# Performance work log

Hardware: AMD Instinct MI355X
Metric: run time of the kernel (lower is better)

Reference implementation:

```python
import jax, jax.numpy as jnp
import numpy as np
from jax import lax

SIGMA = 1.0
ALPHA = 1.0
BETA = 1.0
TRUNCATE = 4.0  # scipy.ndimage default


def _gauss_kernel(sigma):
    radius = int(TRUNCATE * sigma + 0.5)  # scipy radius rule -> 4 for sigma=1
    x = np.arange(-radius, radius + 1, dtype=np.float64)
    k = np.exp(-0.5 * (x / sigma) ** 2)
    k = (k / k.sum()).astype(np.float32)
    return k

_KERNEL = _gauss_kernel(SIGMA)


def _blur_axis(img, k, axis):
    # scipy mode='reflect' == jnp.pad mode='symmetric' (edge repeated)
    r = len(k) // 2
    pad = [(0, 0)] * img.ndim
    pad[axis] = (r, r)
    xp = jnp.pad(img, pad, mode='symmetric')
    n = img.shape[axis]
    out = k[0] * lax.slice_in_dim(xp, 0, n, axis=axis)
    for i in range(1, len(k)):
        out = out + k[i] * lax.slice_in_dim(xp, i, i + n, axis=axis)
    return out


def gaussian_blur(img):
    # scalar sigma in scipy blurs along EVERY axis, including batch & channel
    k = jnp.asarray(_KERNEL, dtype=img.dtype)
    for ax in range(img.ndim):
        img = _blur_axis(img, k, ax)
    return img


def decompose(I):
    I_log = jnp.log(I + 1e-6)
    I_smooth = gaussian_blur(I_log)
    R = I_log - I_smooth
    L = I_log - R  # == I_smooth
    return jnp.exp(L), jnp.exp(R)


def setup_inputs() -> dict:
    key = jax.random.key(0)
    k1, k2 = jax.random.split(key)
    shape = (16, 3, 512, 512)
    I_enhanced = jax.random.uniform(k1, shape, dtype=jnp.float32)
    I_gt = jax.random.uniform(k2, shape, dtype=jnp.float32)
    return {"I_enhanced": I_enhanced, "I_gt": I_gt}


def reference(I_enhanced, I_gt):
    L_enh, R_enh = decompose(I_enhanced)
    L_gt, R_gt = decompose(I_gt)
    L_reflectance = jnp.mean((R_enh - R_gt) ** 2)
    L_illumination = jnp.mean((L_enh - L_gt) ** 2)
    return ALPHA * L_reflectance + BETA * L_illumination
```

## Files before the change

### kernel.cpp

```cpp
#include <hip/hip_runtime.h>
#include <hip/hip_fp16.h>
#include <cmath>

#define PLANE (512*512)
#define NPLANES 48
#define NEL (48*PLANE)

struct Taps { float k[9]; };
struct CMat { float w[3][3]; };


__global__ __launch_bounds__(64)
void k_blur_hw(const float* __restrict__ inE, const float* __restrict__ inG,
               ushort* __restrict__ wsS, ushort* __restrict__ wsI, Taps tp)
{
    const int l    = threadIdx.x;
    const int w0   = (blockIdx.x & 1) * 256;
    const int r0   = (blockIdx.x >> 1) * 32;
    const int z    = blockIdx.y;

    const float* src = (z < NPLANES) ? (inE + z * PLANE)
                                     : (inG + (z - NPLANES) * PLANE);

    const int  col   = w0 + 4 * l;
    const bool is0   = (l == 0);
    const bool is63  = (l == 63);
    const bool ledge = (w0 == 0);
    const bool redge = (w0 + 256 == 512);
    const bool do_halo = (is0 && !ledge) || (is63 && !redge);
    const int  hoff  = is0 ? (w0 - 4) : (w0 + 256);
    const int  tile  = col >> 6;
    const int  inner = col & 63;

    __half2 kh[9];
#pragma unroll
    for (int t = 0; t < 9; ++t) kh[t] = __float2half2_rn(tp.k[t]);

    __half2 ring[10][2];

#define FOLD(r) ((r) < 0 ? (-1 - (r)) : ((r) > 511 ? (1023 - (r)) : (r)))

    float4 pown[3], phal[3];
    phal[0] = phal[1] = phal[2] = make_float4(1.f, 1.f, 1.f, 1.f);
#pragma unroll
    for (int s = 0; s < 3; ++s) {
        const float* rp = src + FOLD(r0 - 4 + s) * 512;
        pown[s] = *(const float4*)(rp + col);
        if (do_halo) phal[s] = *(const float4*)(rp + hoff);
    }

    for (int jb = 0; jb < 40; jb += 10) {
#pragma unroll
        for (int u = 0; u < 10; ++u) {
            const int j = jb + u;

            float4 own = pown[0], hal = phal[0];
            pown[0] = pown[1]; pown[1] = pown[2];
            phal[0] = phal[1]; phal[1] = phal[2];
            if (j + 3 < 40) {
                const float* rp = src + FOLD(r0 - 1 + j) * 512;
                pown[2] = *(const float4*)(rp + col);
                if (do_halo) phal[2] = *(const float4*)(rp + hoff);
            }

            if (j >= 4 && j < 36) {
                const int ri = r0 + j - 4;
                __half2 i0 = __floats2half2_rn(own.x + 1e-6f, own.y + 1e-6f);
                __half2 i1 = __floats2half2_rn(own.z + 1e-6f, own.w + 1e-6f);
                ushort* dpI = wsI + (((ri * 8 + tile) * 96) + z) * 64 + inner;
                *(uint2*)dpI = make_uint2(*(uint*)&i0, *(uint*)&i1);
            }

            const float w4 = __logf(own.x + 1e-6f);
            const float w5 = __logf(own.y + 1e-6f);
            const float w6 = __logf(own.z + 1e-6f);
            const float w7 = __logf(own.w + 1e-6f);
            const float h0 = __logf(hal.x + 1e-6f);
            const float h1 = __logf(hal.y + 1e-6f);
            const float h2 = __logf(hal.z + 1e-6f);
            const float h3 = __logf(hal.w + 1e-6f);

            float win[12];
            win[4] = w4; win[5] = w5; win[6] = w6; win[7] = w7;
            win[0] = __shfl_up(w4, 1);
            win[1] = __shfl_up(w5, 1);
            win[2] = __shfl_up(w6, 1);
            win[3] = __shfl_up(w7, 1);
            win[8]  = __shfl_down(w4, 1);
            win[9]  = __shfl_down(w5, 1);
            win[10] = __shfl_down(w6, 1);
            win[11] = __shfl_down(w7, 1);
            if (is0) {
                if (ledge) { win[0] = w7; win[1] = w6; win[2] = w5; win[3] = w4; }
                else       { win[0] = h0; win[1] = h1; win[2] = h2; win[3] = h3; }
            }
            if (is63) {
                if (redge) { win[8] = w7; win[9] = w6; win[10] = w5; win[11] = w4; }
                else       { win[8] = h0; win[9] = h1; win[10] = h2; win[11] = h3; }
            }

            {
                float o0 = 0.f, o1 = 0.f, o2 = 0.f, o3 = 0.f;
#pragma unroll
                for (int t = 0; t < 9; ++t) {
                    const float kt = tp.k[t];
                    o0 += kt * win[t];
                    o1 += kt * win[t + 1];
                    o2 += kt * win[t + 2];
                    o3 += kt * win[t + 3];
                }
                ring[u][0] = __floats2half2_rn(o0, o1);
                ring[u][1] = __floats2half2_rn(o2, o3);
            }

            if (j >= 8) {
                __half2 a0 = __float2half2_rn(0.f), a1 = a0;
#pragma unroll
                for (int t = 0; t < 9; ++t) {
                    const int sl = (u + 2 + t) % 10;
                    a0 = __hfma2(kh[t], ring[sl][0], a0);
                    a1 = __hfma2(kh[t], ring[sl][1], a1);
                }
                const int ro = r0 + j - 8;
                ushort* dpS = wsS + (((ro * 8 + tile) * 96) + z) * 64 + inner;
                *(uint2*)dpS = make_uint2(*(uint*)&a0, *(uint*)&a1);
            }
        }
    }
#undef FOLD
}

__global__ __launch_bounds__(256)
void k_cn_loss(const ushort* __restrict__ wsS, const ushort* __restrict__ wsI,
               float* __restrict__ out, Taps tp, CMat cm)
{
    const int tid = threadIdx.x;
    const int P   = blockIdx.x * 256 + tid;
    const int hw0 = P * 2;
    const int off = (hw0 >> 6) * (96 * 64) + (hw0 & 63);
    const ushort* sbase = wsS + off;
    const ushort* ibase = wsI + off;

    __half2 k2[9], cw[3][3];
#pragma unroll
    for (int t = 0; t < 9; ++t) k2[t] = __float2half2_rn(tp.k[t]);
#pragma unroll
    for (int i = 0; i < 3; ++i)
#pragma unroll
        for (int j = 0; j < 3; ++j) cw[i][j] = __float2half2_rn(cm.w[i][j]);

    __half2 re[9][3];
    __half2 rg[9][3];

#define LOADRAW(m, uE, uG)                                                     \
    uE[0] = *(const uint*)(sbase + ((m) * 3 + 0) * 64);                        \
    uE[1] = *(const uint*)(sbase + ((m) * 3 + 1) * 64);                        \
    uE[2] = *(const uint*)(sbase + ((m) * 3 + 2) * 64);                        \
    uG[0] = *(const uint*)(sbase + (48 + (m) * 3 + 0) * 64);                   \
    uG[1] = *(const uint*)(sbase + (48 + (m) * 3 + 1) * 64);                   \
    uG[2] = *(const uint*)(sbase + (48 + (m) * 3 + 2) * 64);

#define CBLUR(u, dst)                                                          \
    {                                                                          \
        __half2 v0 = *(__half2*)&u[0];                                         \
        __half2 v1 = *(__half2*)&u[1];                                         \
        __half2 v2 = *(__half2*)&u[2];                                         \
        dst[0] = __hfma2(cw[0][0], v0, __hfma2(cw[0][1], v1, __hmul2(cw[0][2], v2))); \
        dst[1] = __hfma2(cw[1][0], v0, __hfma2(cw[1][1], v1, __hmul2(cw[1][2], v2))); \
        dst[2] = __hfma2(cw[2][0], v0, __hfma2(cw[2][1], v1, __hmul2(cw[2][2], v2))); \
    }

#pragma unroll
    for (int m = 0; m < 4; ++m) {
        uint uE[3], uG[3];
        LOADRAW(m, uE, uG);
        CBLUR(uE, re[m]); CBLUR(uG, rg[m]);
    }
    uint nuE[3], nuG[3];
    LOADRAW(4, nuE, nuG);
    uint ieq[3], igq[3];
#pragma unroll
    for (int c = 0; c < 3; ++c) {
        ieq[c] = *(const uint*)(ibase + c * 64);
        igq[c] = *(const uint*)(ibase + (48 + c) * 64);
    }

    float acc = 0.f;
#pragma unroll
    for (int n = 0; n < 16; ++n) {
        uint nie[3], nig[3];
        if (n + 1 < 16) {
#pragma unroll
            for (int c = 0; c < 3; ++c) {
                nie[c] = *(const uint*)(ibase + (((n + 1) * 3 + c)) * 64);
                nig[c] = *(const uint*)(ibase + ((48 + (n + 1) * 3 + c)) * 64);
            }
        }
        const int mnew = n + 4;
        if (mnew < 16) {
            CBLUR(nuE, re[mnew % 9]); CBLUR(nuG, rg[mnew % 9]);
            if (mnew + 1 < 16) { LOADRAW(mnew + 1, nuE, nuG); }
        }
#pragma unroll
        for (int c = 0; c < 3; ++c) {
            __half2 se2 = __float2half2_rn(0.f), sg2 = se2;
#pragma unroll
            for (int t = 0; t < 9; ++t) {
                int m = n - 4 + t;
                m = (m < 0) ? (-1 - m) : ((m > 15) ? (31 - m) : m);
                se2 = __hfma2(k2[t], re[m % 9][c], se2);
                sg2 = __hfma2(k2[t], rg[m % 9][c], sg2);
            }
            const float2 sef = __half22float2(se2);
            const float2 sgf = __half22float2(sg2);
            const float2 ief = __half22float2(*(__half2*)&ieq[c]);
            const float2 igf = __half22float2(*(__half2*)&igq[c]);

            {
                float ee = __expf(-sef.x), eg = __expf(-sgf.x);
                float Re = ief.x * ee;
                float Rg = igf.x * eg;
                float Le = __builtin_amdgcn_rcpf(ee);
                float Lg = __builtin_amdgcn_rcpf(eg);
                float dr = Re - Rg, dl = Le - Lg;
                acc += dr * dr + dl * dl;
            }
            {
                float ee = __expf(-sef.y), eg = __expf(-sgf.y);
                float Re = ief.y * ee;
                float Rg = igf.y * eg;
                float Le = __builtin_amdgcn_rcpf(ee);
                float Lg = __builtin_amdgcn_rcpf(eg);
                float dr = Re - Rg, dl = Le - Lg;
                acc += dr * dr + dl * dl;
            }
        }
        if (n + 1 < 16) {
#pragma unroll
            for (int c = 0; c < 3; ++c) { ieq[c] = nie[c]; igq[c] = nig[c]; }
        }
    }
#undef LOADRAW
#undef CBLUR

    __shared__ float red[256];
    red[tid] = acc;
    __syncthreads();
#pragma unroll
    for (int s = 128; s > 0; s >>= 1) {
        if (tid < s) red[tid] += red[tid + s];
        __syncthreads();
    }
    if (tid == 0) atomicAdd(out, red[0] * (1.0f / (float)NEL));
}

extern "C" void kernel_launch(void* const* d_in, const int* in_sizes, int n_in,
                              void* d_out, int out_size, void* d_ws, size_t ws_size,
                              hipStream_t stream) {
    const float* Ie = (const float*)d_in[0];
    const float* Ig = (const float*)d_in[1];

    Taps tp;
    {
        double kk[9], s = 0.0;
        for (int i = 0; i < 9; ++i) { double x = (double)(i - 4); kk[i] = exp(-0.5 * x * x); s += kk[i]; }
        for (int i = 0; i < 9; ++i) tp.k[i] = (float)(kk[i] / s);
    }

    CMat cm;
    {
        for (int c = 0; c < 3; ++c) {
            cm.w[c][0] = cm.w[c][1] = cm.w[c][2] = 0.f;
            for (int t = 0; t < 9; ++t) {
                int m = c - 4 + t;
                int mm = ((m % 6) + 6) % 6;
                if (mm > 2) mm = 5 - mm;
                cm.w[c][mm] += tp.k[t];
            }
        }
    }

    ushort* wsS = (ushort*)d_ws;
    ushort* wsI = wsS + 2 * (size_t)NEL;

    hipMemsetAsync(d_out, 0, sizeof(float), stream);
    dim3 g1(32, 96);
    k_blur_hw<<<g1, 64, 0, stream>>>(Ie, Ig, wsS, wsI, tp);
    k_cn_loss<<<512, 256, 0, stream>>>(wsS, wsI, (float*)d_out, tp, cm);
}
```

Before: 166.3 us.

## Pair enhanced/gt values in half2 and share row halos via LDS

The first kernel now processes the enhanced and ground-truth planes together, with 128 threads covering a full 512-wide row and 16 rows per block. Horizontal neighbours are exchanged through double-buffered shared memory instead of shuffles and separately loaded halo columns. Workspace entries pack the E and G values of one pixel into a single half2, so the loss kernel does one load and one blur per pair and maps one thread per pixel over twice as many blocks. This removes the redundant halo loads and the duplicated E/G address streams, at the cost of a __syncthreads per row and shorter row strips, which add more vertical halo rows per block.

```diff
diff --git a/kernel.cpp b/kernel.cpp
--- a/kernel.cpp
+++ b/kernel.cpp
@@ -10,136 +10,152 @@
 struct CMat { float w[3][3]; };
 
 
-__global__ __launch_bounds__(64)
+#define FOLD(r) ((r) < 0 ? (-1 - (r)) : ((r) > 511 ? (1023 - (r)) : (r)))
+
+__global__ __launch_bounds__(128)
 void k_blur_hw(const float* __restrict__ inE, const float* __restrict__ inG,
-               ushort* __restrict__ wsS, ushort* __restrict__ wsI, Taps tp)
+               uint* __restrict__ wsS, uint* __restrict__ wsI, Taps tp)
 {
-    const int l    = threadIdx.x;
-    const int w0   = (blockIdx.x & 1) * 256;
-    const int r0   = (blockIdx.x >> 1) * 32;
-    const int z    = blockIdx.y;
-
-    const float* src = (z < NPLANES) ? (inE + z * PLANE)
-                                     : (inG + (z - NPLANES) * PLANE);
-
-    const int  col   = w0 + 4 * l;
-    const bool is0   = (l == 0);
-    const bool is63  = (l == 63);
-    const bool ledge = (w0 == 0);
-    const bool redge = (w0 + 256 == 512);
-    const bool do_halo = (is0 && !ledge) || (is63 && !redge);
-    const int  hoff  = is0 ? (w0 - 4) : (w0 + 256);
-    const int  tile  = col >> 6;
-    const int  inner = col & 63;
+    const int g  = threadIdx.x;
+    const int r0 = blockIdx.x * 16;
+    const int z  = blockIdx.y;
+    const float* __restrict__ srcE = inE + z * PLANE;
+    const float* __restrict__ srcG = inG + z * PLANE;
+    const int col   = 4 * g;
+    const int tile  = col >> 6;
+    const int inner = col & 63;
+    const bool edge = (g == 0) || (g == 127);
+    const int  eoff = (g == 0) ? 0 : 516;
+
+    __shared__ float buf[2][2][520];
 
     __half2 kh[9];
 #pragma unroll
     for (int t = 0; t < 9; ++t) kh[t] = __float2half2_rn(tp.k[t]);
 
-    __half2 ring[10][2];
-
-#define FOLD(r) ((r) < 0 ? (-1 - (r)) : ((r) > 511 ? (1023 - (r)) : (r)))
-
-    float4 pown[3], phal[3];
-    phal[0] = phal[1] = phal[2] = make_float4(1.f, 1.f, 1.f, 1.f);
+    __half2 ring[12][4];
+
+    float4 pE[3], pG[3];
 #pragma unroll
     for (int s = 0; s < 3; ++s) {
-        const float* rp = src + FOLD(r0 - 4 + s) * 512;
-        pown[s] = *(const float4*)(rp + col);
-        if (do_halo) phal[s] = *(const float4*)(rp + hoff);
-    }
-
-    for (int jb = 0; jb < 40; jb += 10) {
-#pragma unroll
-        for (int u = 0; u < 10; ++u) {
-            const int j = jb + u;
-
-            float4 own = pown[0], hal = phal[0];
-            pown[0] = pown[1]; pown[1] = pown[2];
-            phal[0] = phal[1]; phal[1] = phal[2];
-            if (j + 3 < 40) {
-                const float* rp = src + FOLD(r0 - 1 + j) * 512;
-                pown[2] = *(const float4*)(rp + col);
-                if (do_halo) phal[2] = *(const float4*)(rp + hoff);
-            }
-
-            if (j >= 4 && j < 36) {
+        const int row = FOLD(r0 - 4 + s);
+        pE[s] = *(const float4*)(srcE + row * 512 + col);
+        pG[s] = *(const float4*)(srcG + row * 512 + col);
+    }
+
+#pragma unroll
+    for (int jb = 0; jb < 24; jb += 12) {
+#pragma unroll
+        for (int u = 0; u < 12; ++u) {
+            const int j   = jb + u;
+            const int par = j & 1;
+
+            float4 oe = pE[0], og = pG[0];
+            pE[0] = pE[1]; pE[1] = pE[2];
+            pG[0] = pG[1]; pG[1] = pG[2];
+            if (j + 3 < 24) {
+                const int row = FOLD(r0 - 1 + j);
+                pE[2] = *(const float4*)(srcE + row * 512 + col);
+                pG[2] = *(const float4*)(srcG + row * 512 + col);
+            }
+
+            const float e4 = __logf(oe.x + 1e-6f);
+            const float e5 = __logf(oe.y + 1e-6f);
+            const float e6 = __logf(oe.z + 1e-6f);
+            const float e7 = __logf(oe.w + 1e-6f);
+            const float g4 = __logf(og.x + 1e-6f);
+            const float g5 = __logf(og.y + 1e-6f);
+            const float g6 = __logf(og.z + 1e-6f);
+            const float g7 = __logf(og.w + 1e-6f);
+
+            *(float4*)&buf[par][0][4 + col] = make_float4(e4, e5, e6, e7);
+            *(float4*)&buf[par][1][4 + col] = make_float4(g4, g5, g6, g7);
+            if (edge) {
+                *(float4*)&buf[par][0][eoff] = make_float4(e7, e6, e5, e4);
+                *(float4*)&buf[par][1][eoff] = make_float4(g7, g6, g5, g4);
+            }
+
+            if (j >= 4 && j < 20) {
                 const int ri = r0 + j - 4;
-                __half2 i0 = __floats2half2_rn(own.x + 1e-6f, own.y + 1e-6f);
-                __half2 i1 = __floats2half2_rn(own.z + 1e-6f, own.w + 1e-6f);
-                ushort* dpI = wsI + (((ri * 8 + tile) * 96) + z) * 64 + inner;
-                *(uint2*)dpI = make_uint2(*(uint*)&i0, *(uint*)&i1);
-            }
-
-            const float w4 = __logf(own.x + 1e-6f);
-            const float w5 = __logf(own.y + 1e-6f);
-            const float w6 = __logf(own.z + 1e-6f);
-            const float w7 = __logf(own.w + 1e-6f);
-            const float h0 = __logf(hal.x + 1e-6f);
-            const float h1 = __logf(hal.y + 1e-6f);
-            const float h2 = __logf(hal.z + 1e-6f);
-            const float h3 = __logf(hal.w + 1e-6f);
-
-            float win[12];
-            win[4] = w4; win[5] = w5; win[6] = w6; win[7] = w7;
-            win[0] = __shfl_up(w4, 1);
-            win[1] = __shfl_up(w5, 1);
-            win[2] = __shfl_up(w6, 1);
-            win[3] = __shfl_up(w7, 1);
-            win[8]  = __shfl_down(w4, 1);
-            win[9]  = __shfl_down(w5, 1);
-            win[10] = __shfl_down(w6, 1);
-            win[11] = __shfl_down(w7, 1);
-            if (is0) {
-                if (ledge) { win[0] = w7; win[1] = w6; win[2] = w5; win[3] = w4; }
-                else       { win[0] = h0; win[1] = h1; win[2] = h2; win[3] = h3; }
-            }
-            if (is63) {
-                if (redge) { win[8] = w7; win[9] = w6; win[10] = w5; win[11] = w4; }
-                else       { win[8] = h0; win[9] = h1; win[10] = h2; win[11] = h3; }
-            }
-
+                __half2 i0 = __floats2half2_rn(oe.x + 1e-6f, og.x + 1e-6f);
+                __half2 i1 = __floats2half2_rn(oe.y + 1e-6f, og.y + 1e-6f);
+                __half2 i2 = __floats2half2_rn(oe.z + 1e-6f, og.z + 1e-6f);
+                __half2 i3 = __floats2half2_rn(oe.w + 1e-6f, og.w + 1e-6f);
+                uint* dp = wsI + (((ri * 8 + tile) * 48) + z) * 64 + inner;
+                *(uint4*)dp = make_uint4(*(uint*)&i0, *(uint*)&i1,
+                                         *(uint*)&i2, *(uint*)&i3);
+            }
+
+            __syncthreads();
+
+            float oE0, oE1, oE2, oE3, oG0, oG1, oG2, oG3;
             {
+                float4 lA = *(const float4*)&buf[par][0][col];
+                float4 lB = *(const float4*)&buf[par][0][col + 8];
+                float wv[12] = {lA.x, lA.y, lA.z, lA.w, e4, e5, e6, e7,
+                                lB.x, lB.y, lB.z, lB.w};
                 float o0 = 0.f, o1 = 0.f, o2 = 0.f, o3 = 0.f;
 #pragma unroll
                 for (int t = 0; t < 9; ++t) {
                     const float kt = tp.k[t];
-                    o0 += kt * win[t];
-                    o1 += kt * win[t + 1];
-                    o2 += kt * win[t + 2];
-                    o3 += kt * win[t + 3];
+                    o0 += kt * wv[t];
+                    o1 += kt * wv[t + 1];
+                    o2 += kt * wv[t + 2];
+                    o3 += kt * wv[t + 3];
                 }
-                ring[u][0] = __floats2half2_rn(o0, o1);
-                ring[u][1] = __floats2half2_rn(o2, o3);
-            }
+                oE0 = o0; oE1 = o1; oE2 = o2; oE3 = o3;
+            }
+            {
+                float4 lA = *(const float4*)&buf[par][1][col];
+                float4 lB = *(const float4*)&buf[par][1][col + 8];
+                float wv[12] = {lA.x, lA.y, lA.z, lA.w, g4, g5, g6, g7,
+                                lB.x, lB.y, lB.z, lB.w};
+                float o0 = 0.f, o1 = 0.f, o2 = 0.f, o3 = 0.f;
+#pragma unroll
+                for (int t = 0; t < 9; ++t) {
+                    const float kt = tp.k[t];
+                    o0 += kt * wv[t];
+                    o1 += kt * wv[t + 1];
+                    o2 += kt * wv[t + 2];
+                    o3 += kt * wv[t + 3];
+                }
+                oG0 = o0; oG1 = o1; oG2 = o2; oG3 = o3;
+            }
+            ring[u][0] = __floats2half2_rn(oE0, oG0);
+            ring[u][1] = __floats2half2_rn(oE1, oG1);
+            ring[u][2] = __floats2half2_rn(oE2, oG2);
+            ring[u][3] = __floats2half2_rn(oE3, oG3);
 
             if (j >= 8) {
-                __half2 a0 = __float2half2_rn(0.f), a1 = a0;
+                __half2 a0 = __float2half2_rn(0.f), a1 = a0, a2 = a0, a3 = a0;
 #pragma unroll
                 for (int t = 0; t < 9; ++t) {
-                    const int sl = (u + 2 + t) % 10;
+                    const int sl = (j - 8 + t) % 12;
                     a0 = __hfma2(kh[t], ring[sl][0], a0);
                     a1 = __hfma2(kh[t], ring[sl][1], a1);
+                    a2 = __hfma2(kh[t], ring[sl][2], a2);
+                    a3 = __hfma2(kh[t], ring[sl][3], a3);
                 }
                 const int ro = r0 + j - 8;
-                ushort* dpS = wsS + (((ro * 8 + tile) * 96) + z) * 64 + inner;
-                *(uint2*)dpS = make_uint2(*(uint*)&a0, *(uint*)&a1);
-            }
-        }
-    }
-#undef FOLD
+                uint* dp = wsS + (((ro * 8 + tile) * 48) + z) * 64 + inner;
+                *(uint4*)dp = make_uint4(*(uint*)&a0, *(uint*)&a1,
+                                         *(uint*)&a2, *(uint*)&a3);
+            }
+        }
+    }
 }
 
 __global__ __launch_bounds__(256)
-void k_cn_loss(const ushort* __restrict__ wsS, const ushort* __restrict__ wsI,
+void k_cn_loss(const uint* __restrict__ wsS, const uint* __restrict__ wsI,
                float* __restrict__ out, Taps tp, CMat cm)
 {
     const int tid = threadIdx.x;
-    const int P   = blockIdx.x * 256 + tid;
-    const int hw0 = P * 2;
-    const int off = (hw0 >> 6) * (96 * 64) + (hw0 & 63);
-    const ushort* sbase = wsS + off;
-    const ushort* ibase = wsI + off;
+    const int p   = blockIdx.x * 256 + tid;
+    const int w   = p & 511;
+    const int h   = p >> 9;
+    const int base = ((h * 8 + (w >> 6)) * 48) * 64 + (w & 63);
+    const uint* __restrict__ sb = wsS + base;
+    const uint* __restrict__ ib = wsI + base;
 
     __half2 k2[9], cw[3][3];
 #pragma unroll
@@ -147,100 +163,71 @@
 #pragma unroll
     for (int i = 0; i < 3; ++i)
 #pragma unroll
-        for (int j = 0; j < 3; ++j) cw[i][j] = __float2half2_rn(cm.w[i][j]);
-
-    __half2 re[9][3];
-    __half2 rg[9][3];
-
-#define LOADRAW(m, uE, uG)                                                     \
-    uE[0] = *(const uint*)(sbase + ((m) * 3 + 0) * 64);                        \
-    uE[1] = *(const uint*)(sbase + ((m) * 3 + 1) * 64);                        \
-    uE[2] = *(const uint*)(sbase + ((m) * 3 + 2) * 64);                        \
-    uG[0] = *(const uint*)(sbase + (48 + (m) * 3 + 0) * 64);                   \
-    uG[1] = *(const uint*)(sbase + (48 + (m) * 3 + 1) * 64);                   \
-    uG[2] = *(const uint*)(sbase + (48 + (m) * 3 + 2) * 64);
-
-#define CBLUR(u, dst)                                                          \
+        for (int jj = 0; jj < 3; ++jj) cw[i][jj] = __float2half2_rn(cm.w[i][jj]);
+
+    __half2 r[9][3];
+
+#define LOADS(m, u)                                                            \
+    u[0] = sb[((m) * 3 + 0) * 64];                                             \
+    u[1] = sb[((m) * 3 + 1) * 64];                                             \
+    u[2] = sb[((m) * 3 + 2) * 64];
+
+#define CBLUR(u, d)                                                            \
     {                                                                          \
         __half2 v0 = *(__half2*)&u[0];                                         \
         __half2 v1 = *(__half2*)&u[1];                                         \
         __half2 v2 = *(__half2*)&u[2];                                         \
-        dst[0] = __hfma2(cw[0][0], v0, __hfma2(cw[0][1], v1, __hmul2(cw[0][2], v2))); \
-        dst[1] = __hfma2(cw[1][0], v0, __hfma2(cw[1][1], v1, __hmul2(cw[1][2], v2))); \
-        dst[2] = __hfma2(cw[2][0], v0, __hfma2(cw[2][1], v1, __hmul2(cw[2][2], v2))); \
-    }
-
-#pragma unroll
-    for (int m = 0; m < 4; ++m) {
-        uint uE[3], uG[3];
-        LOADRAW(m, uE, uG);
-        CBLUR(uE, re[m]); CBLUR(uG, rg[m]);
-    }
-    uint nuE[3], nuG[3];
-    LOADRAW(4, nuE, nuG);
-    uint ieq[3], igq[3];
-#pragma unroll
-    for (int c = 0; c < 3; ++c) {
-        ieq[c] = *(const uint*)(ibase + c * 64);
-        igq[c] = *(const uint*)(ibase + (48 + c) * 64);
-    }
+        d[0] = __hfma2(cw[0][0], v0, __hfma2(cw[0][1], v1, __hmul2(cw[0][2], v2))); \
+        d[1] = __hfma2(cw[1][0], v0, __hfma2(cw[1][1], v1, __hmul2(cw[1][2], v2))); \
+        d[2] = __hfma2(cw[2][0], v0, __hfma2(cw[2][1], v1, __hmul2(cw[2][2], v2))); \
+    }
+
+    {
+        uint su[3];
+#pragma unroll
+        for (int m = 0; m < 4; ++m) { LOADS(m, su); CBLUR(su, r[m]); }
+    }
+    uint nu[3];
+    LOADS(4, nu);
+    uint iu[3];
+    iu[0] = ib[0]; iu[1] = ib[64]; iu[2] = ib[128];
 
     float acc = 0.f;
 #pragma unroll
     for (int n = 0; n < 16; ++n) {
-        uint nie[3], nig[3];
+        uint niu[3];
         if (n + 1 < 16) {
 #pragma unroll
-            for (int c = 0; c < 3; ++c) {
-                nie[c] = *(const uint*)(ibase + (((n + 1) * 3 + c)) * 64);
-                nig[c] = *(const uint*)(ibase + ((48 + (n + 1) * 3 + c)) * 64);
-            }
+            for (int c = 0; c < 3; ++c) niu[c] = ib[((n + 1) * 3 + c) * 64];
         }
         const int mnew = n + 4;
         if (mnew < 16) {
-            CBLUR(nuE, re[mnew % 9]); CBLUR(nuG, rg[mnew % 9]);
-            if (mnew + 1 < 16) { LOADRAW(mnew + 1, nuE, nuG); }
+            CBLUR(nu, r[mnew % 9]);
+            if (mnew + 1 < 16) { LOADS(mnew + 1, nu); }
         }
 #pragma unroll
         for (int c = 0; c < 3; ++c) {
-            __half2 se2 = __float2half2_rn(0.f), sg2 = se2;
+            __half2 s2 = __float2half2_rn(0.f);
 #pragma unroll
             for (int t = 0; t < 9; ++t) {
                 int m = n - 4 + t;
                 m = (m < 0) ? (-1 - m) : ((m > 15) ? (31 - m) : m);
-                se2 = __hfma2(k2[t], re[m % 9][c], se2);
-                sg2 = __hfma2(k2[t], rg[m % 9][c], sg2);
-            }
-            const float2 sef = __half22float2(se2);
-            const float2 sgf = __half22float2(sg2);
-            const float2 ief = __half22float2(*(__half2*)&ieq[c]);
-            const float2 igf = __half22float2(*(__half2*)&igq[c]);
-
-            {
-                float ee = __expf(-sef.x), eg = __expf(-sgf.x);
-                float Re = ief.x * ee;
-                float Rg = igf.x * eg;
-                float Le = __builtin_amdgcn_rcpf(ee);
-                float Lg = __builtin_amdgcn_rcpf(eg);
-                float dr = Re - Rg, dl = Le - Lg;
-                acc += dr * dr + dl * dl;
-            }
-            {
-                float ee = __expf(-sef.y), eg = __expf(-sgf.y);
-                float Re = ief.y * ee;
-                float Rg = igf.y * eg;
-                float Le = __builtin_amdgcn_rcpf(ee);
-                float Lg = __builtin_amdgcn_rcpf(eg);
-                float dr = Re - Rg, dl = Le - Lg;
-                acc += dr * dr + dl * dl;
-            }
-        }
-        if (n + 1 < 16) {
-#pragma unroll
-            for (int c = 0; c < 3; ++c) { ieq[c] = nie[c]; igq[c] = nig[c]; }
-        }
-    }
-#undef LOADRAW
+                s2 = __hfma2(k2[t], r[m % 9][c], s2);
+            }
+            const float2 sf  = __half22float2(s2);
+            const float2 if2 = __half22float2(*(__half2*)&iu[c]);
+
+            float eE = __expf(-sf.x), eG = __expf(-sf.y);
+            float Re = if2.x * eE;
+            float Rg = if2.y * eG;
+            float Le = __builtin_amdgcn_rcpf(eE);
+            float Lg = __builtin_amdgcn_rcpf(eG);
+            float dr = Re - Rg, dl = Le - Lg;
+            acc += dr * dr + dl * dl;
+        }
+        if (n + 1 < 16) { iu[0] = niu[0]; iu[1] = niu[1]; iu[2] = niu[2]; }
+    }
+#undef LOADS
 #undef CBLUR
 
     __shared__ float red[256];
@@ -280,11 +267,11 @@
         }
     }
 
-    ushort* wsS = (ushort*)d_ws;
-    ushort* wsI = wsS + 2 * (size_t)NEL;
+    uint* wsS = (uint*)d_ws;
+    uint* wsI = wsS + (size_t)NEL;
 
     hipMemsetAsync(d_out, 0, sizeof(float), stream);
-    dim3 g1(32, 96);
-    k_blur_hw<<<g1, 64, 0, stream>>>(Ie, Ig, wsS, wsI, tp);
-    k_cn_loss<<<512, 256, 0, stream>>>(wsS, wsI, (float*)d_out, tp, cm);
+    dim3 g1(32, 48);
+    k_blur_hw<<<g1, 128, 0, stream>>>(Ie, Ig, wsS, wsI, tp);
+    k_cn_loss<<<1024, 256, 0, stream>>>(wsS, wsI, (float*)d_out, tp, cm);
 }
```

Result: slower. 176.8 us (+6.3%).

## Restructure HW blur: full-row wavefront, 8 columns per lane, packed half2 horizontal pass

Applied to the files above, without the earlier changes.

The horizontal+vertical blur kernel now has one wavefront cover a full 512-wide row, with 8 columns per lane. This removes the halo loads and the two-half-row split, and row strips shrink from 32 to 16 rows. The horizontal 9-tap pass now runs in packed half2 on log values. Neighbour values are assembled by shuffling and bit-repacking half pairs, with lane pairs interleaving columns c and c+4. Stores widen to 16 bytes. In exchange, the vertical halo is re-read more often because strips are shorter, the horizontal pass loses precision in fp16, and edge reflection depends on bit-manipulation packing that has to be correct.

```diff
diff --git a/kernel.cpp b/kernel.cpp
--- a/kernel.cpp
+++ b/kernel.cpp
@@ -9,125 +9,130 @@
 struct Taps { float k[9]; };
 struct CMat { float w[3][3]; };
 
+
+#define FOLD(r) ((r) < 0 ? (-1 - (r)) : ((r) > 511 ? (1023 - (r)) : (r)))
 
 __global__ __launch_bounds__(64)
 void k_blur_hw(const float* __restrict__ inE, const float* __restrict__ inG,
                ushort* __restrict__ wsS, ushort* __restrict__ wsI, Taps tp)
 {
-    const int l    = threadIdx.x;
-    const int w0   = (blockIdx.x & 1) * 256;
-    const int r0   = (blockIdx.x >> 1) * 32;
-    const int z    = blockIdx.y;
-
-    const float* src = (z < NPLANES) ? (inE + z * PLANE)
-                                     : (inG + (z - NPLANES) * PLANE);
-
-    const int  col   = w0 + 4 * l;
-    const bool is0   = (l == 0);
-    const bool is63  = (l == 63);
-    const bool ledge = (w0 == 0);
-    const bool redge = (w0 + 256 == 512);
-    const bool do_halo = (is0 && !ledge) || (is63 && !redge);
-    const int  hoff  = is0 ? (w0 - 4) : (w0 + 256);
-    const int  tile  = col >> 6;
-    const int  inner = col & 63;
+    const int l  = threadIdx.x;
+    const int r0 = blockIdx.x * 16;
+    const int z  = blockIdx.y;
+    const float* __restrict__ src = (z < NPLANES) ? (inE + z * PLANE)
+                                                  : (inG + (z - NPLANES) * PLANE);
+    const int col  = 8 * l;
+    const int tile = l >> 3;
+    const int sh   = (l & 7) * 8;
 
     __half2 kh[9];
 #pragma unroll
     for (int t = 0; t < 9; ++t) kh[t] = __float2half2_rn(tp.k[t]);
 
-    __half2 ring[10][2];
-
-#define FOLD(r) ((r) < 0 ? (-1 - (r)) : ((r) > 511 ? (1023 - (r)) : (r)))
-
-    float4 pown[3], phal[3];
-    phal[0] = phal[1] = phal[2] = make_float4(1.f, 1.f, 1.f, 1.f);
+    uint ring[12][4];
+
+    float4 pA[3], pB[3];
 #pragma unroll
     for (int s = 0; s < 3; ++s) {
-        const float* rp = src + FOLD(r0 - 4 + s) * 512;
-        pown[s] = *(const float4*)(rp + col);
-        if (do_halo) phal[s] = *(const float4*)(rp + hoff);
-    }
-
-    for (int jb = 0; jb < 40; jb += 10) {
-#pragma unroll
-        for (int u = 0; u < 10; ++u) {
+        const int row = FOLD(r0 - 4 + s);
+        pA[s] = *(const float4*)(src + row * 512 + col);
+        pB[s] = *(const float4*)(src + row * 512 + col + 4);
+    }
+
+    for (int jb = 0; jb < 24; jb += 12) {
+#pragma unroll
+        for (int u = 0; u < 12; ++u) {
             const int j = jb + u;
 
-            float4 own = pown[0], hal = phal[0];
-            pown[0] = pown[1]; pown[1] = pown[2];
-            phal[0] = phal[1]; phal[1] = phal[2];
-            if (j + 3 < 40) {
-                const float* rp = src + FOLD(r0 - 1 + j) * 512;
-                pown[2] = *(const float4*)(rp + col);
-                if (do_halo) phal[2] = *(const float4*)(rp + hoff);
-            }
-
-            if (j >= 4 && j < 36) {
+            const float4 a = pA[0], b = pB[0];
+            pA[0] = pA[1]; pA[1] = pA[2];
+            pB[0] = pB[1]; pB[1] = pB[2];
+            if (j + 3 < 24) {
+                const int row = FOLD(r0 - 1 + j);
+                pA[2] = *(const float4*)(src + row * 512 + col);
+                pB[2] = *(const float4*)(src + row * 512 + col + 4);
+            }
+
+            const float a0 = a.x + 1e-6f, a1 = a.y + 1e-6f;
+            const float a2 = a.z + 1e-6f, a3 = a.w + 1e-6f;
+            const float b0 = b.x + 1e-6f, b1 = b.y + 1e-6f;
+            const float b2 = b.z + 1e-6f, b3 = b.w + 1e-6f;
+
+            if (j >= 4 && j < 20) {
                 const int ri = r0 + j - 4;
-                __half2 i0 = __floats2half2_rn(own.x + 1e-6f, own.y + 1e-6f);
-                __half2 i1 = __floats2half2_rn(own.z + 1e-6f, own.w + 1e-6f);
-                ushort* dpI = wsI + (((ri * 8 + tile) * 96) + z) * 64 + inner;
-                *(uint2*)dpI = make_uint2(*(uint*)&i0, *(uint*)&i1);
-            }
-
-            const float w4 = __logf(own.x + 1e-6f);
-            const float w5 = __logf(own.y + 1e-6f);
-            const float w6 = __logf(own.z + 1e-6f);
-            const float w7 = __logf(own.w + 1e-6f);
-            const float h0 = __logf(hal.x + 1e-6f);
-            const float h1 = __logf(hal.y + 1e-6f);
-            const float h2 = __logf(hal.z + 1e-6f);
-            const float h3 = __logf(hal.w + 1e-6f);
-
-            float win[12];
-            win[4] = w4; win[5] = w5; win[6] = w6; win[7] = w7;
-            win[0] = __shfl_up(w4, 1);
-            win[1] = __shfl_up(w5, 1);
-            win[2] = __shfl_up(w6, 1);
-            win[3] = __shfl_up(w7, 1);
-            win[8]  = __shfl_down(w4, 1);
-            win[9]  = __shfl_down(w5, 1);
-            win[10] = __shfl_down(w6, 1);
-            win[11] = __shfl_down(w7, 1);
-            if (is0) {
-                if (ledge) { win[0] = w7; win[1] = w6; win[2] = w5; win[3] = w4; }
-                else       { win[0] = h0; win[1] = h1; win[2] = h2; win[3] = h3; }
-            }
-            if (is63) {
-                if (redge) { win[8] = w7; win[9] = w6; win[10] = w5; win[11] = w4; }
-                else       { win[8] = h0; win[9] = h1; win[10] = h2; win[11] = h3; }
-            }
-
+                __half2 i0 = __floats2half2_rn(a0, b0);
+                __half2 i1 = __floats2half2_rn(a1, b1);
+                __half2 i2 = __floats2half2_rn(a2, b2);
+                __half2 i3 = __floats2half2_rn(a3, b3);
+                ushort* dpI = wsI + (((ri * 8 + tile) * 96) + z) * 64 + sh;
+                *(uint4*)dpI = make_uint4(*(uint*)&i0, *(uint*)&i1,
+                                          *(uint*)&i2, *(uint*)&i3);
+            }
+
+            uint c[4];
             {
-                float o0 = 0.f, o1 = 0.f, o2 = 0.f, o3 = 0.f;
-#pragma unroll
-                for (int t = 0; t < 9; ++t) {
-                    const float kt = tp.k[t];
-                    o0 += kt * win[t];
-                    o1 += kt * win[t + 1];
-                    o2 += kt * win[t + 2];
-                    o3 += kt * win[t + 3];
+                __half2 h0 = __floats2half2_rn(__logf(a0), __logf(b0));
+                __half2 h1 = __floats2half2_rn(__logf(a1), __logf(b1));
+                __half2 h2 = __floats2half2_rn(__logf(a2), __logf(b2));
+                __half2 h3 = __floats2half2_rn(__logf(a3), __logf(b3));
+                c[0] = *(uint*)&h0; c[1] = *(uint*)&h1;
+                c[2] = *(uint*)&h2; c[3] = *(uint*)&h3;
+            }
+
+            uint wpk[12];
+#pragma unroll
+            for (int i = 0; i < 4; ++i) {
+                const uint up = (uint)__shfl_up((int)c[i], 1);
+                const uint dn = (uint)__shfl_down((int)c[i], 1);
+                wpk[i]     = (up >> 16) | (c[i] << 16);
+                wpk[4 + i] = c[i];
+                wpk[8 + i] = (c[i] >> 16) | (dn << 16);
+            }
+            if (l == 0) {
+#pragma unroll
+                for (int x = 0; x < 4; ++x)
+                    wpk[x] = (c[3 - x] & 0xffffu) | (c[x] << 16);
+            }
+            if (l == 63) {
+                wpk[8]  = (c[0] >> 16) | (c[3] & 0xffff0000u);
+                wpk[9]  = (c[1] >> 16) | (c[2] & 0xffff0000u);
+                wpk[10] = (c[2] >> 16) | (c[1] & 0xffff0000u);
+                wpk[11] = (c[3] >> 16) | (c[0] & 0xffff0000u);
+            }
+
+#pragma unroll
+            for (int i = 0; i < 4; ++i) {
+                __half2 acc = __hmul2(kh[0], *(__half2*)&wpk[i]);
+#pragma unroll
+                for (int t = 1; t < 9; ++t)
+                    acc = __hfma2(kh[t], *(__half2*)&wpk[i + t], acc);
+                ring[u][i] = *(uint*)&acc;
+            }
+
+            if (j >= 8) {
+                __half2 s0, s1, s2, s3;
+                {
+                    const int sl = (u + 4) % 12;
+                    s0 = __hmul2(kh[0], *(__half2*)&ring[sl][0]);
+                    s1 = __hmul2(kh[0], *(__half2*)&ring[sl][1]);
+                    s2 = __hmul2(kh[0], *(__half2*)&ring[sl][2]);
+                    s3 = __hmul2(kh[0], *(__half2*)&ring[sl][3]);
                 }
-                ring[u][0] = __floats2half2_rn(o0, o1);
-                ring[u][1] = __floats2half2_rn(o2, o3);
-            }
-
-            if (j >= 8) {
-                __half2 a0 = __float2half2_rn(0.f), a1 = a0;
-#pragma unroll
-                for (int t = 0; t < 9; ++t) {
-                    const int sl = (u + 2 + t) % 10;
-                    a0 = __hfma2(kh[t], ring[sl][0], a0);
-                    a1 = __hfma2(kh[t], ring[sl][1], a1);
+#pragma unroll
+                for (int t = 1; t < 9; ++t) {
+                    const int sl = (u + 4 + t) % 12;
+                    s0 = __hfma2(kh[t], *(__half2*)&ring[sl][0], s0);
+                    s1 = __hfma2(kh[t], *(__half2*)&ring[sl][1], s1);
+                    s2 = __hfma2(kh[t], *(__half2*)&ring[sl][2], s2);
+                    s3 = __hfma2(kh[t], *(__half2*)&ring[sl][3], s3);
                 }
                 const int ro = r0 + j - 8;
-                ushort* dpS = wsS + (((ro * 8 + tile) * 96) + z) * 64 + inner;
-                *(uint2*)dpS = make_uint2(*(uint*)&a0, *(uint*)&a1);
-            }
-        }
-    }
-#undef FOLD
+                ushort* dpS = wsS + (((ro * 8 + tile) * 96) + z) * 64 + sh;
+                *(uint4*)dpS = make_uint4(*(uint*)&s0, *(uint*)&s1,
+                                          *(uint*)&s2, *(uint*)&s3);
+            }
+        }
+    }
 }
 
 __global__ __launch_bounds__(256)
```

Result: no change. 163.4 us (-1.8%).
